# Kernel tuning notes

Hardware: AMD Instinct MI355X
Metric: run time of the kernel (lower is better)

## Reference

```python
import jax, jax.numpy as jnp
import numpy as np

T, C, H = 4096, 1024, 16
D = C // H  # head dim = 64


def setup_inputs() -> dict:
    key = jax.random.key(0)
    k1, k2, k3 = jax.random.split(key, 3)
    x = jax.random.normal(k1, (T, C), dtype=jnp.float32)
    w_attn = jax.random.normal(k2, (C, 3 * C), dtype=jnp.float32) * (1.0 / np.sqrt(C))
    w_proj = jax.random.normal(k3, (C, C), dtype=jnp.float32) * (1.0 / np.sqrt(C))
    return {"x": x, "w_attn": w_attn, "w_proj": w_proj, "num_frames": 64}


def reference(x, w_attn, w_proj, num_frames):
    t, c = x.shape
    d = c // H
    qkv = x @ w_attn                       # (T, 3C)
    q, k, v = jnp.split(qkv, 3, axis=-1)   # each (T, C)
    # (T, H, D) -> (H, T, D)
    q = q.reshape(t, H, d).transpose(1, 0, 2)
    k = k.reshape(t, H, d).transpose(1, 0, 2)
    v = v.reshape(t, H, d).transpose(1, 0, 2)
    # causal mask with dense global prefix: every query may attend to the
    # first num_frames keys in addition to the causal lower triangle.
    rows = jnp.arange(t)[:, None]
    cols = jnp.arange(t)[None, :]
    mask = (cols <= rows) | (cols < num_frames)   # (T, T) bool
    scores = jnp.einsum('htd,hsd->hts', q, k) * (1.0 / np.sqrt(d))  # (H,T,T)
    scores = jnp.where(mask[None], scores, jnp.float32(-jnp.inf))
    att = jax.nn.softmax(scores, axis=-1)
    y = jnp.einsum('hts,hsd->htd', att, v)        # (H, T, D)
    y = y.transpose(1, 0, 2).reshape(t, c)        # (T, C)
    return y @ w_proj
```

## Files before the change

kernel.cpp:

```cpp
#include <hip/hip_runtime.h>
#include <hip/hip_bf16.h>

#define Tq 4096
#define Cdim 1024
#define NH 16
#define DH 64

typedef __attribute__((ext_vector_type(8))) short short8;
typedef __attribute__((ext_vector_type(4))) float f32x4;

__device__ __forceinline__ unsigned short f2bf(float f) {
  union { float f; unsigned int u; } v; v.f = f;
  unsigned int r = v.u + 0x7FFFu + ((v.u >> 16) & 1u);
  return (unsigned short)(r >> 16);
}

__device__ __forceinline__ unsigned int cvtpk_bf16(float lo, float hi) {
  unsigned int r;
  asm volatile("v_cvt_pk_bf16_f32 %0, %1, %2" : "=v"(r) : "v"(lo), "v"(hi));
  return r;
}

__global__ void cvt_kernel(const float* __restrict__ in, unsigned short* __restrict__ out, int n) {
  int idx = (blockIdx.x * blockDim.x + threadIdx.x) * 4;
  if (idx + 3 < n) {
    float4 v = *reinterpret_cast<const float4*>(in + idx);
    ushort4 o;
    o.x = f2bf(v.x); o.y = f2bf(v.y); o.z = f2bf(v.z); o.w = f2bf(v.w);
    *reinterpret_cast<ushort4*>(out + idx) = o;
  }
}

__global__ void transpose_cvt(const float* __restrict__ in, unsigned short* __restrict__ out,
                              int R, int Ccols) {
  __shared__ float tile[64][65];
  int c0 = blockIdx.x * 64, r0 = blockIdx.y * 64;
  int tx = threadIdx.x & 63;
  int ty = threadIdx.x >> 6;
  #pragma unroll
  for (int rr = 0; rr < 64; rr += 4)
    tile[rr + ty][tx] = in[(r0 + rr + ty) * Ccols + c0 + tx];
  __syncthreads();
  #pragma unroll
  for (int rr = 0; rr < 64; rr += 4)
    out[(c0 + rr + ty) * R + r0 + tx] = f2bf(tile[tx][rr + ty]);
}

template<int OUT_MODE>
__global__ __launch_bounds__(256, 3)
void gemm_bt(const unsigned short* __restrict__ A,
             const unsigned short* __restrict__ B,
             void* __restrict__ Cout,
             int M, int N, int K)
{
  __shared__ __align__(16) unsigned short As[128][64];
  __shared__ __align__(16) unsigned short Bs[128][64];
  const int tid = threadIdx.x;
  const int lane = tid & 63;
  const int wave = tid >> 6;
  const int wm = wave >> 1, wn = wave & 1;

  const int chunk = gridDim.x >> 3;
  const int b = blockIdx.x;
  const int swz = (b & 7) * chunk + (b >> 3);
  const int n0 = (swz >> 5) * 128;
  const int m0 = (swz & 31) * 128;

  f32x4 acc[4][4] = {};

  const int lrow = lane >> 3;
  const int lcol = (lane & 7) * 8;

  for (int k0 = 0; k0 < K; k0 += 64) {
    __syncthreads();
    #pragma unroll
    for (int t = 0; t < 4; ++t) {
      const int r = wave * 32 + t * 8;
      __builtin_amdgcn_global_load_lds(
        (const __attribute__((address_space(1))) void*)&A[(size_t)(m0 + r + lrow) * K + k0 + lcol],
        (__attribute__((address_space(3))) void*)&As[r][0], 16, 0, 0);
      __builtin_amdgcn_global_load_lds(
        (const __attribute__((address_space(1))) void*)&B[(size_t)(n0 + r + lrow) * K + k0 + lcol],
        (__attribute__((address_space(3))) void*)&Bs[r][0], 16, 0, 0);
    }
    __syncthreads();
    #pragma unroll
    for (int kk = 0; kk < 64; kk += 32) {
      const int frow = lane & 15;
      const int fcol = kk + 8 * (lane >> 4);
      short8 a[4], bfr[4];
      #pragma unroll
      for (int i = 0; i < 4; ++i) {
        a[i]   = *reinterpret_cast<const short8*>(&As[wm * 64 + i * 16 + frow][fcol]);
        bfr[i] = *reinterpret_cast<const short8*>(&Bs[wn * 64 + i * 16 + frow][fcol]);
      }
      #pragma unroll
      for (int i = 0; i < 4; ++i)
        #pragma unroll
        for (int j = 0; j < 4; ++j)
          acc[i][j] = __builtin_amdgcn_mfma_f32_16x16x32_bf16(a[i], bfr[j], acc[i][j], 0, 0, 0);
    }
  }

  const int rbase = (lane >> 4) * 4;
  const int ccol = lane & 15;
  #pragma unroll
  for (int i = 0; i < 4; ++i) {
    const int row0 = m0 + wm * 64 + i * 16 + rbase;
    #pragma unroll
    for (int j = 0; j < 4; ++j) {
      const int col = n0 + wn * 64 + j * 16 + ccol;
      if (OUT_MODE == 0) {
        unsigned short* q = (unsigned short*)Cout;
        int sec = col >> 10, rem = col & 1023;
        int hh = rem >> 6, d = rem & 63;
        if (sec == 2) {
          ushort4 pk;
          pk.x = f2bf(acc[i][j][0]); pk.y = f2bf(acc[i][j][1]);
          pk.z = f2bf(acc[i][j][2]); pk.w = f2bf(acc[i][j][3]);
          *reinterpret_cast<ushort4*>(
              &q[((size_t)(2 * NH + hh) * DH + d) * Tq + row0]) = pk;
        } else {
          #pragma unroll
          for (int r = 0; r < 4; ++r)
            q[(((size_t)sec * NH + hh) * Tq + row0 + r) * DH + d] = f2bf(acc[i][j][r]);
        }
      } else {
        #pragma unroll
        for (int r = 0; r < 4; ++r)
          ((float*)Cout)[(row0 + r) * N + col] = acc[i][j][r];
      }
    }
  }
}

__global__ __launch_bounds__(256, 4)
void attn_kernel(const unsigned short* __restrict__ qkv,
                 unsigned short* __restrict__ y,
                 const int* __restrict__ nf_ptr)
{
  __shared__ __align__(16) unsigned short Ks[128][72];
  __shared__ __align__(16) unsigned short VTs[64][136];

  const int tid  = threadIdx.x;
  const int lane = tid & 63;
  const int w    = tid >> 6;
  const int g    = lane >> 4;
  const int li   = lane & 15;

  const int h  = blockIdx.x & 15;
  const int iq = (blockIdx.x >> 4) & 31;
  const int hi = blockIdx.x >> 9;
  const int qc = hi ? iq : 63 - iq;
  const int q0 = qc * 64;
  const int nf = nf_ptr[0];

  const unsigned short* Qh  = qkv + (size_t)h * Tq * DH;
  const unsigned short* Kh  = qkv + (size_t)(NH + h) * Tq * DH;
  const unsigned short* VTh = qkv + (size_t)(2 * NH + h) * DH * Tq;

  const int qrow = q0 + w * 16 + li;
  short8 qf[2];
  #pragma unroll
  for (int kk = 0; kk < 2; ++kk)
    qf[kk] = *reinterpret_cast<const short8*>(&Qh[qrow * DH + kk * 32 + 8 * g]);

  f32x4 o[4] = {};
  f32x4 ol = {};

  short8 ones;
  #pragma unroll
  for (int e = 0; e < 8; ++e) ones[e] = (short)0x3F80;

  int lastt = q0 + 63;
  if (nf - 1 > lastt) lastt = nf - 1;
  const int ktend = lastt >> 7;

  const float SCL = 0.125f * 1.44269504f;
  const float M0  = 12.0f;

  const int krow0 = tid >> 3;
  const int kcol  = (tid & 7) * 8;
  const int vrow0 = tid >> 4;
  const int vcol  = (tid & 15) * 8;

  {
    short8 nk[4], nv[4];
    #pragma unroll
    for (int j = 0; j < 4; ++j) {
      nk[j] = *reinterpret_cast<const short8*>(&Kh[(krow0 + 32 * j) * DH + kcol]);
      nv[j] = *reinterpret_cast<const short8*>(&VTh[(size_t)(vrow0 + 16 * j) * Tq + vcol]);
    }
    #pragma unroll
    for (int j = 0; j < 4; ++j) {
      *reinterpret_cast<short8*>(&Ks[krow0 + 32 * j][kcol]) = nk[j];
      *reinterpret_cast<short8*>(&VTs[vrow0 + 16 * j][vcol]) = nv[j];
    }
  }
  __syncthreads();

  for (int kt = 0; kt <= ktend; ++kt) {
    const int kv0 = kt * 128;
    const bool havenext = (kt < ktend);
    short8 nk[4], nv[4];
    if (havenext) {
      const int nx = kv0 + 128;
      #pragma unroll
      for (int j = 0; j < 4; ++j) {
        nk[j] = *reinterpret_cast<const short8*>(&Kh[(nx + krow0 + 32 * j) * DH + kcol]);
        nv[j] = *reinterpret_cast<const short8*>(&VTh[(size_t)(vrow0 + 16 * j) * Tq + nx + vcol]);
      }
    }

    #pragma unroll
    for (int h2 = 0; h2 < 2; ++h2) {
      const int kvb = kv0 + h2 * 64;

      f32x4 s[4];
      __builtin_amdgcn_s_setprio(1);
      #pragma unroll
      for (int nb = 0; nb < 4; ++nb) {
        f32x4 a = {};
        #pragma unroll
        for (int kk = 0; kk < 2; ++kk) {
          short8 kf = *reinterpret_cast<const short8*>(
              &Ks[h2 * 64 + nb * 16 + li][kk * 32 + 8 * g]);
          a = __builtin_amdgcn_mfma_f32_16x16x32_bf16(kf, qf[kk], a, 0, 0, 0);
        }
        s[nb] = a;
      }
      __builtin_amdgcn_s_setprio(0);

      const bool needmask = !((kvb + 63 <= q0 + w * 16) || (kvb + 63 < nf));
      float p[4][4];
      #pragma unroll
      for (int nb = 0; nb < 4; ++nb) {
        #pragma unroll
        for (int r = 0; r < 4; ++r) {
          float v = s[nb][r];
          if (needmask) {
            const int kvi = kvb + nb * 16 + 4 * g + r;
            if (!(kvi <= qrow || kvi < nf)) v = -1e30f;
          }
          p[nb][r] = exp2f(__builtin_fmaf(v, SCL, -M0));
        }
      }

      #pragma unroll
      for (int kk = 0; kk < 2; ++kk) {
        unsigned int X1 = cvtpk_bf16(p[2 * kk][0], p[2 * kk][1]);
        unsigned int X2 = cvtpk_bf16(p[2 * kk][2], p[2 * kk][3]);
        unsigned int Y1 = cvtpk_bf16(p[2 * kk + 1][0], p[2 * kk + 1][1]);
        unsigned int Y2 = cvtpk_bf16(p[2 * kk + 1][2], p[2 * kk + 1][3]);
        asm volatile("v_permlane32_swap_b32 %0, %1" : "+v"(X1), "+v"(Y1));
        asm volatile("v_permlane32_swap_b32 %0, %1" : "+v"(X2), "+v"(Y2));
        asm volatile("v_permlane16_swap_b32 %0, %1" : "+v"(X1), "+v"(Y1));
        asm volatile("v_permlane16_swap_b32 %0, %1" : "+v"(X2), "+v"(Y2));
        union { unsigned int u[4]; short8 s8; } W;
        W.u[0] = X1; W.u[1] = X2; W.u[2] = Y1; W.u[3] = Y2;
        __builtin_amdgcn_s_setprio(1);
        #pragma unroll
        for (int db = 0; db < 4; ++db) {
          short8 vb = *reinterpret_cast<const short8*>(
              &VTs[db * 16 + li][h2 * 64 + kk * 32 + 8 * g]);
          o[db] = __builtin_amdgcn_mfma_f32_16x16x32_bf16(vb, W.s8, o[db], 0, 0, 0);
        }
        ol = __builtin_amdgcn_mfma_f32_16x16x32_bf16(ones, W.s8, ol, 0, 0, 0);
        __builtin_amdgcn_s_setprio(0);
      }
    }

    if (havenext) {
      __syncthreads();
      #pragma unroll
      for (int j = 0; j < 4; ++j) {
        *reinterpret_cast<short8*>(&Ks[krow0 + 32 * j][kcol]) = nk[j];
        *reinterpret_cast<short8*>(&VTs[vrow0 + 16 * j][vcol]) = nv[j];
      }
      __syncthreads();
    }
  }

  const float inv = 1.0f / ol[0];
  unsigned short* yp = y + (size_t)qrow * Cdim + h * DH;
  #pragma unroll
  for (int db = 0; db < 4; ++db) {
    ushort4 pk;
    pk.x = f2bf(o[db][0] * inv);
    pk.y = f2bf(o[db][1] * inv);
    pk.z = f2bf(o[db][2] * inv);
    pk.w = f2bf(o[db][3] * inv);
    *reinterpret_cast<ushort4*>(&yp[db * 16 + 4 * g]) = pk;
  }
}

extern "C" void kernel_launch(void* const* d_in, const int* in_sizes, int n_in,
                              void* d_out, int out_size, void* d_ws, size_t ws_size,
                              hipStream_t stream) {
  (void)in_sizes; (void)n_in; (void)out_size; (void)ws_size;
  const float* x  = (const float*)d_in[0];
  const float* wa = (const float*)d_in[1];
  const float* wp = (const float*)d_in[2];
  const int*   nf = (const int*)d_in[3];
  float* out = (float*)d_out;

  char* ws = (char*)d_ws;
  unsigned short* x_bf = (unsigned short*)(ws);
  unsigned short* waT  = (unsigned short*)(ws + (size_t)8  * 1024 * 1024);
  unsigned short* wpT  = (unsigned short*)(ws + (size_t)14 * 1024 * 1024);
  unsigned short* qkvb = (unsigned short*)(ws + (size_t)16 * 1024 * 1024);
  unsigned short* ybf  = (unsigned short*)(ws + (size_t)40 * 1024 * 1024);

  cvt_kernel<<<4096, 256, 0, stream>>>(x, x_bf, Tq * Cdim);
  transpose_cvt<<<dim3(48, 16), 256, 0, stream>>>(wa, waT, 1024, 3072);
  transpose_cvt<<<dim3(16, 16), 256, 0, stream>>>(wp, wpT, 1024, 1024);
  gemm_bt<0><<<768, 256, 0, stream>>>(x_bf, waT, (void*)qkvb, Tq, 3 * Cdim, Cdim);
  attn_kernel<<<1024, 256, 0, stream>>>(qkvb, ybf, nf);
  gemm_bt<1><<<256, 256, 0, stream>>>(ybf, wpT, (void*)out, Tq, Cdim, Cdim);
}
```

Before: 161.0 us.

## Split attention KV range across two blocks and merge partials in new kernel

Each (head, query-chunk) attention block is split in two. One block handles the even 128-key tiles and the other the odd ones, so twice as many blocks launch, ordered heaviest-first. Each block writes unnormalized bf16 partial outputs and fp32 row sums, with the partials staged in the output buffer and the sums in the workspace. A new merge kernel adds the two partials and divides by the combined sum to produce y. This aims to raise occupancy and balance the long causal rows, at the cost of an extra launch, extra global traffic and bf16 rounding of the partials.

```diff
diff --git a/kernel.cpp b/kernel.cpp
--- a/kernel.cpp
+++ b/kernel.cpp
@@ -13,6 +13,11 @@
   union { float f; unsigned int u; } v; v.f = f;
   unsigned int r = v.u + 0x7FFFu + ((v.u >> 16) & 1u);
   return (unsigned short)(r >> 16);
+}
+
+__device__ __forceinline__ float bf2f(unsigned short u) {
+  union { unsigned int u; float f; } v; v.u = ((unsigned int)u) << 16;
+  return v.f;
 }
 
 __device__ __forceinline__ unsigned int cvtpk_bf16(float lo, float hi) {
@@ -136,7 +141,8 @@
 
 __global__ __launch_bounds__(256, 4)
 void attn_kernel(const unsigned short* __restrict__ qkv,
-                 unsigned short* __restrict__ y,
+                 unsigned short* __restrict__ po,
+                 float* __restrict__ pl,
                  const int* __restrict__ nf_ptr)
 {
   __shared__ __align__(16) unsigned short Ks[128][72];
@@ -149,9 +155,8 @@
   const int li   = lane & 15;
 
   const int h  = blockIdx.x & 15;
-  const int iq = (blockIdx.x >> 4) & 31;
-  const int hi = blockIdx.x >> 9;
-  const int qc = hi ? iq : 63 - iq;
+  const int s  = (blockIdx.x >> 4) & 1;
+  const int qc = 63 - (blockIdx.x >> 5);
   const int q0 = qc * 64;
   const int nf = nf_ptr[0];
 
@@ -174,7 +179,7 @@
 
   int lastt = q0 + 63;
   if (nf - 1 > lastt) lastt = nf - 1;
-  const int ktend = lastt >> 7;
+  const int T = (lastt >> 7) + 1;
 
   const float SCL = 0.125f * 1.44269504f;
   const float M0  = 12.0f;
@@ -185,11 +190,12 @@
   const int vcol  = (tid & 15) * 8;
 
   {
+    const int nx = s * 128;
     short8 nk[4], nv[4];
     #pragma unroll
     for (int j = 0; j < 4; ++j) {
-      nk[j] = *reinterpret_cast<const short8*>(&Kh[(krow0 + 32 * j) * DH + kcol]);
-      nv[j] = *reinterpret_cast<const short8*>(&VTh[(size_t)(vrow0 + 16 * j) * Tq + vcol]);
+      nk[j] = *reinterpret_cast<const short8*>(&Kh[(nx + krow0 + 32 * j) * DH + kcol]);
+      nv[j] = *reinterpret_cast<const short8*>(&VTh[(size_t)(vrow0 + 16 * j) * Tq + nx + vcol]);
     }
     #pragma unroll
     for (int j = 0; j < 4; ++j) {
@@ -199,12 +205,12 @@
   }
   __syncthreads();
 
-  for (int kt = 0; kt <= ktend; ++kt) {
-    const int kv0 = kt * 128;
-    const bool havenext = (kt < ktend);
+  for (int t = s; t < T; t += 2) {
+    const int kv0 = t * 128;
+    const bool havenext = (t + 2 < T);
     short8 nk[4], nv[4];
     if (havenext) {
-      const int nx = kv0 + 128;
+      const int nx = kv0 + 256;
       #pragma unroll
       for (int j = 0; j < 4; ++j) {
         nk[j] = *reinterpret_cast<const short8*>(&Kh[(nx + krow0 + 32 * j) * DH + kcol]);
@@ -216,7 +222,7 @@
     for (int h2 = 0; h2 < 2; ++h2) {
       const int kvb = kv0 + h2 * 64;
 
-      f32x4 s[4];
+      f32x4 sarr[4];
       __builtin_amdgcn_s_setprio(1);
       #pragma unroll
       for (int nb = 0; nb < 4; ++nb) {
@@ -227,7 +233,7 @@
               &Ks[h2 * 64 + nb * 16 + li][kk * 32 + 8 * g]);
           a = __builtin_amdgcn_mfma_f32_16x16x32_bf16(kf, qf[kk], a, 0, 0, 0);
         }
-        s[nb] = a;
+        sarr[nb] = a;
       }
       __builtin_amdgcn_s_setprio(0);
 
@@ -237,7 +243,7 @@
       for (int nb = 0; nb < 4; ++nb) {
         #pragma unroll
         for (int r = 0; r < 4; ++r) {
-          float v = s[nb][r];
+          float v = sarr[nb][r];
           if (needmask) {
             const int kvi = kvb + nb * 16 + 4 * g + r;
             if (!(kvi <= qrow || kvi < nf)) v = -1e30f;
@@ -281,17 +287,42 @@
     }
   }
 
-  const float inv = 1.0f / ol[0];
-  unsigned short* yp = y + (size_t)qrow * Cdim + h * DH;
+  unsigned short* pp = po + (((size_t)s * NH + h) * Tq + qrow) * DH;
   #pragma unroll
   for (int db = 0; db < 4; ++db) {
     ushort4 pk;
-    pk.x = f2bf(o[db][0] * inv);
-    pk.y = f2bf(o[db][1] * inv);
-    pk.z = f2bf(o[db][2] * inv);
-    pk.w = f2bf(o[db][3] * inv);
-    *reinterpret_cast<ushort4*>(&yp[db * 16 + 4 * g]) = pk;
-  }
+    pk.x = f2bf(o[db][0]);
+    pk.y = f2bf(o[db][1]);
+    pk.z = f2bf(o[db][2]);
+    pk.w = f2bf(o[db][3]);
+    *reinterpret_cast<ushort4*>(&pp[db * 16 + 4 * g]) = pk;
+  }
+  if (g == 0)
+    pl[((size_t)s * NH + h) * Tq + qrow] = ol[0];
+}
+
+__global__ __launch_bounds__(256)
+void merge_kernel(const unsigned short* __restrict__ po,
+                  const float* __restrict__ pl,
+                  unsigned short* __restrict__ ybf)
+{
+  const int idx = blockIdx.x * 256 + threadIdx.x;
+  const int d8  = idx & 7;
+  const int row = (idx >> 3) & 4095;
+  const int h   = idx >> 15;
+  const size_t base = ((size_t)h * Tq + row) * DH + d8 * 8;
+  short8 a = *reinterpret_cast<const short8*>(&po[base]);
+  short8 b = *reinterpret_cast<const short8*>(&po[(size_t)NH * Tq * DH + base]);
+  const float l0 = pl[(size_t)h * Tq + row];
+  const float l1 = pl[(size_t)NH * Tq + (size_t)h * Tq + row];
+  const float inv = 1.0f / (l0 + l1);
+  short8 outv;
+  #pragma unroll
+  for (int j = 0; j < 8; ++j) {
+    float v = (bf2f((unsigned short)a[j]) + bf2f((unsigned short)b[j])) * inv;
+    outv[j] = (short)f2bf(v);
+  }
+  *reinterpret_cast<short8*>(&ybf[(size_t)row * Cdim + h * DH + d8 * 8]) = outv;
 }
 
 extern "C" void kernel_launch(void* const* d_in, const int* in_sizes, int n_in,
@@ -311,10 +342,14 @@
   unsigned short* qkvb = (unsigned short*)(ws + (size_t)16 * 1024 * 1024);
   unsigned short* ybf  = (unsigned short*)(ws + (size_t)40 * 1024 * 1024);
 
+  unsigned short* po = (unsigned short*)d_out;
+  float* pl = (float*)(ws);
+
   cvt_kernel<<<4096, 256, 0, stream>>>(x, x_bf, Tq * Cdim);
   transpose_cvt<<<dim3(48, 16), 256, 0, stream>>>(wa, waT, 1024, 3072);
   transpose_cvt<<<dim3(16, 16), 256, 0, stream>>>(wp, wpT, 1024, 1024);
   gemm_bt<0><<<768, 256, 0, stream>>>(x_bf, waT, (void*)qkvb, Tq, 3 * Cdim, Cdim);
-  attn_kernel<<<1024, 256, 0, stream>>>(qkvb, ybf, nf);
+  attn_kernel<<<2048, 256, 0, stream>>>(qkvb, po, pl, nf);
+  merge_kernel<<<2048, 256, 0, stream>>>(po, pl, ybf);
   gemm_bt<1><<<256, 256, 0, stream>>>(ybf, wpT, (void*)out, Tq, Cdim, Cdim);
 }
```

Result: faster. 152.5 us (-5.3%).
